# Kernel optimization log

Hardware: AMD Instinct MI355X
Metric: run time of the kernel (lower is better)

The kernel has to match this reference:

```python
import jax, jax.numpy as jnp
import numpy as np

B, N, XDIM, EDIM, H = 4, 256, 256, 128, 8
DF = XDIM // H


def _linear_params(key, din, dout):
    k1, k2 = jax.random.split(key)
    s = 1.0 / np.sqrt(din)
    W = jax.random.uniform(k1, (din, dout), minval=-s, maxval=s, dtype=jnp.float32)
    b = jax.random.uniform(k2, (dout,), minval=-s, maxval=s, dtype=jnp.float32)
    return W, b


def setup_inputs() -> dict:
    key = jax.random.key(0)
    ks = jax.random.split(key, 9)
    x = jax.random.normal(ks[0], (B, N, XDIM), dtype=jnp.float32)
    e = jax.random.normal(ks[1], (B, N, N, EDIM), dtype=jnp.float32)
    Wq, bq = _linear_params(ks[2], XDIM, XDIM)
    Wk, bk = _linear_params(ks[3], XDIM, XDIM)
    Wv, bv = _linear_params(ks[4], XDIM, XDIM)
    Wem, bem = _linear_params(ks[5], EDIM, XDIM)  # e_mul
    Wea, bea = _linear_params(ks[6], EDIM, XDIM)  # e_add
    Wxo, bxo = _linear_params(ks[7], XDIM, XDIM)  # x_out
    Weo, beo = _linear_params(ks[8], XDIM, EDIM)  # e_out
    return {"x": x, "e": e, "Wq": Wq, "bq": bq, "Wk": Wk, "bk": bk,
            "Wv": Wv, "bv": bv, "Wem": Wem, "bem": bem, "Wea": Wea, "bea": bea,
            "Wxo": Wxo, "bxo": bxo, "Weo": Weo, "beo": beo}


def reference(x, e, Wq, bq, Wk, bk, Wv, bv, Wem, bem, Wea, bea, Wxo, bxo, Weo, beo):
    Bq, Nq, _ = x.shape
    # per-node projections -> [B, N, H, DF]
    Q = (x @ Wq + bq).reshape(Bq, Nq, H, DF)
    K = (x @ Wk + bk).reshape(Bq, Nq, H, DF)
    V = (x @ Wv + bv).reshape(Bq, Nq, H, DF)
    # broadcasted outer product: Y[b,i,j,h,d] = Q[b,i,h,d] * K[b,j,h,d] / sqrt(DF)
    Y = Q[:, :, None] * K[:, None] * (1.0 / np.sqrt(DF))  # [B,N,N,H,DF]
    # edge modulation
    E1 = (e @ Wem + bem).reshape(Bq, Nq, Nq, H, DF)
    E2 = (e @ Wea + bea).reshape(Bq, Nq, Nq, H, DF)
    Y = Y * (E1 + 1.0) + E2
    # new edge features
    newE = Y.reshape(Bq, Nq, Nq, XDIM) @ Weo + beo  # [B,N,N,EDIM]
    # attention: softmax over the FIRST node axis (dim=1), as in the torch code
    attn = jax.nn.softmax(Y, axis=1)  # [B,N,N,H,DF]
    # weighted_V[b,j,h,d] = sum_i attn[b,i,j,h,d] * V[b,j,h,d]
    weighted_V = jnp.sum(attn * V[:, None], axis=1)  # [B,N,H,DF]
    newX = weighted_V.reshape(Bq, Nq, XDIM) @ Wxo + bxo  # [B,N,XDIM]
    return (newX, newE)
```

## Files before the change

### kernel.cpp

```cpp
#include <hip/hip_runtime.h>

#define NN 256
#define XD 256
#define ED 128

typedef __attribute__((ext_vector_type(8))) short short8;
typedef __attribute__((ext_vector_type(4))) float f32x4;

__device__ __forceinline__ unsigned short f2bf(float f) {
    unsigned u = __builtin_bit_cast(unsigned, f);
    u += 0x7FFF + ((u >> 16) & 1);
    return (unsigned short)(u >> 16);
}

#define MFMA16(a, b, c) __builtin_amdgcn_mfma_f32_16x16x32_bf16(a, b, c, 0, 0, 0)

__global__ __launch_bounds__(256) void wprep_kernel(
    const float* __restrict__ Wq, const float* __restrict__ Wk,
    const float* __restrict__ Wv, const float* __restrict__ Wxo,
    const float* __restrict__ Wem, const float* __restrict__ Wea,
    const float* __restrict__ Weo,
    short* __restrict__ WqT, short* __restrict__ WkT,
    short* __restrict__ WvT, short* __restrict__ WxoT,
    short* __restrict__ WemT, short* __restrict__ WeaT,
    short* __restrict__ WeoT)
{
    __shared__ float sT[32][33];
    int blk = blockIdx.x;
    const float* src; short* dst; int din, dout, tile;
    if (blk < 256) {
        int m = blk >> 6; tile = blk & 63; din = 256; dout = 256;
        src = m == 0 ? Wq : (m == 1 ? Wk : (m == 2 ? Wv : Wxo));
        dst = m == 0 ? WqT : (m == 1 ? WkT : (m == 2 ? WvT : WxoT));
    } else if (blk < 320) {
        int m = (blk - 256) >> 5; tile = (blk - 256) & 31; din = 128; dout = 256;
        src = m == 0 ? Wem : Wea; dst = m == 0 ? WemT : WeaT;
    } else {
        tile = blk - 320; din = 256; dout = 128;
        src = Weo; dst = WeoT;
    }
    int ksh = (din == 256) ? 3 : 2;
    int kt = tile & ((1 << ksh) - 1);
    int nt = tile >> ksh;
    int c = threadIdx.x & 31, rbase = threadIdx.x >> 5;
    #pragma unroll
    for (int p = 0; p < 4; ++p) {
        int r = rbase + p * 8;
        sT[r][c] = src[(kt * 32 + r) * dout + nt * 32 + c];
    }
    __syncthreads();
    #pragma unroll
    for (int p = 0; p < 4; ++p) {
        int r = rbase + p * 8;
        dst[(nt * 32 + r) * din + kt * 32 + c] = (short)f2bf(sT[c][r]);
    }
}

__global__ __launch_bounds__(512) void proj_qk_kernel(
    const float* __restrict__ x, const short* __restrict__ WqT,
    const short* __restrict__ WkT, const float* __restrict__ bq,
    const float* __restrict__ bk, float* __restrict__ Qs,
    float* __restrict__ KT)
{
    __shared__ unsigned short sX[64 * 264];
    const int blk = blockIdx.x;
    const int mtile = blk >> 1;
    const int mat   = blk & 1;
    const int tid = threadIdx.x, wave = tid >> 6, lane = tid & 63;
    const int quad = lane >> 4, l16 = lane & 15;

    {
        const float4* src4 = (const float4*)(x + (size_t)mtile * 64 * XD);
        #pragma unroll
        for (int it = 0; it < 8; ++it) {
            int idx4 = tid + it * 512;
            float4 v = src4[idx4];
            int elem = idx4 * 4, row = elem >> 8, col = elem & 255;
            short4 p = make_short4((short)f2bf(v.x), (short)f2bf(v.y),
                                   (short)f2bf(v.z), (short)f2bf(v.w));
            *(short4*)&sX[row * 264 + col] = p;
        }
    }
    __syncthreads();

    const short* WT   = mat ? WkT : WqT;
    const float* bias = mat ? bk : bq;
    const int c0 = wave * 32;

    f32x4 acc[4][2] = {};
    for (int ks = 0; ks < 8; ++ks) {
        short8 bfrag[2];
        #pragma unroll
        for (int ct = 0; ct < 2; ++ct)
            bfrag[ct] = *(const short8*)&WT[(c0 + ct * 16 + l16) * 256 + ks * 32 + quad * 8];
        #pragma unroll
        for (int mt = 0; mt < 4; ++mt) {
            short8 a = *(const short8*)&sX[(mt * 16 + l16) * 264 + ks * 32 + quad * 8];
            acc[mt][0] = MFMA16(a, bfrag[0], acc[mt][0]);
            acc[mt][1] = MFMA16(a, bfrag[1], acc[mt][1]);
        }
    }

    if (mat == 0) {
        #pragma unroll
        for (int mt = 0; mt < 4; ++mt)
            #pragma unroll
            for (int ct = 0; ct < 2; ++ct) {
                int cc = c0 + ct * 16 + l16;
                float bb = bias[cc];
                #pragma unroll
                for (int r = 0; r < 4; ++r)
                    Qs[(size_t)(mtile * 64 + mt * 16 + quad * 4 + r) * 256 + cc] =
                        (acc[mt][ct][r] + bb) * 0.17677669529663687f;
            }
    } else {
        int b = mtile >> 2, j0p = (mtile & 3) * 64;
        #pragma unroll
        for (int mt = 0; mt < 4; ++mt)
            #pragma unroll
            for (int ct = 0; ct < 2; ++ct) {
                int cc = c0 + ct * 16 + l16;
                float bb = bias[cc];
                f32x4 st;
                #pragma unroll
                for (int r = 0; r < 4; ++r) st[r] = acc[mt][ct][r] + bb;
                *(f32x4*)&KT[(size_t)(b * 256 + cc) * 256 + j0p + mt * 16 + quad * 4] = st;
            }
    }
}

__global__ __launch_bounds__(512) void proj_vx_kernel(
    const float* __restrict__ x, const short* __restrict__ WvT,
    const float* __restrict__ bv, const short* __restrict__ WxoT,
    const float* __restrict__ bxo, float* __restrict__ outX)
{
    __shared__ unsigned short sX[64 * 264];
    __shared__ unsigned short sV[64 * 264];
    const int mtile = blockIdx.x;
    const int tid = threadIdx.x, wave = tid >> 6, lane = tid & 63;
    const int quad = lane >> 4, l16 = lane & 15;

    {
        const float4* src4 = (const float4*)(x + (size_t)mtile * 64 * XD);
        #pragma unroll
        for (int it = 0; it < 8; ++it) {
            int idx4 = tid + it * 512;
            float4 v = src4[idx4];
            int elem = idx4 * 4, row = elem >> 8, col = elem & 255;
            short4 p = make_short4((short)f2bf(v.x), (short)f2bf(v.y),
                                   (short)f2bf(v.z), (short)f2bf(v.w));
            *(short4*)&sX[row * 264 + col] = p;
        }
    }
    __syncthreads();

    const int c0 = wave * 32;
    f32x4 acc[4][2] = {};
    for (int ks = 0; ks < 8; ++ks) {
        short8 bfrag[2];
        #pragma unroll
        for (int ct = 0; ct < 2; ++ct)
            bfrag[ct] = *(const short8*)&WvT[(c0 + ct * 16 + l16) * 256 + ks * 32 + quad * 8];
        #pragma unroll
        for (int mt = 0; mt < 4; ++mt) {
            short8 a = *(const short8*)&sX[(mt * 16 + l16) * 264 + ks * 32 + quad * 8];
            acc[mt][0] = MFMA16(a, bfrag[0], acc[mt][0]);
            acc[mt][1] = MFMA16(a, bfrag[1], acc[mt][1]);
        }
    }
    #pragma unroll
    for (int mt = 0; mt < 4; ++mt)
        #pragma unroll
        for (int ct = 0; ct < 2; ++ct) {
            int cc = c0 + ct * 16 + l16;
            float bb = bv[cc];
            #pragma unroll
            for (int r = 0; r < 4; ++r)
                sV[(mt * 16 + quad * 4 + r) * 264 + cc] = f2bf(acc[mt][ct][r] + bb);
        }
    __syncthreads();

    f32x4 acc2[4][2] = {};
    for (int ks = 0; ks < 8; ++ks) {
        short8 bfrag[2];
        #pragma unroll
        for (int ct = 0; ct < 2; ++ct)
            bfrag[ct] = *(const short8*)&WxoT[(c0 + ct * 16 + l16) * 256 + ks * 32 + quad * 8];
        #pragma unroll
        for (int mt = 0; mt < 4; ++mt) {
            short8 a = *(const short8*)&sV[(mt * 16 + l16) * 264 + ks * 32 + quad * 8];
            acc2[mt][0] = MFMA16(a, bfrag[0], acc2[mt][0]);
            acc2[mt][1] = MFMA16(a, bfrag[1], acc2[mt][1]);
        }
    }
    #pragma unroll
    for (int mt = 0; mt < 4; ++mt)
        #pragma unroll
        for (int ct = 0; ct < 2; ++ct) {
            int cc = c0 + ct * 16 + l16;
            float bb = bxo[cc];
            #pragma unroll
            for (int r = 0; r < 4; ++r)
                outX[(size_t)(mtile * 64 + mt * 16 + quad * 4 + r) * 256 + cc] =
                    acc2[mt][ct][r] + bb;
        }
}

__global__ __launch_bounds__(256, 3) void fused_edge_kernel(
    const float* __restrict__ e, const float* __restrict__ Qs,
    const float* __restrict__ KT, const short* __restrict__ WemT,
    const short* __restrict__ WeaT, const short* __restrict__ WeoT,
    const float* __restrict__ bem, const float* __restrict__ bea,
    const float* __restrict__ beo, float* __restrict__ outE)
{
    __shared__ unsigned short sE[64 * 140];
    __shared__ unsigned short sY[64 * 268];

    const int blk  = blockIdx.x;
    const int jq   = blk & 3;
    const int i    = (blk >> 2) & 255;
    const int b    = blk >> 10;
    const int j0   = jq * 64;
    const int tid  = threadIdx.x;
    const int wave = tid >> 6;
    const int lane = tid & 63;
    const int quad = lane >> 4;
    const int l16  = lane & 15;

    {
        const float4* src4 = (const float4*)(e + (size_t)((b * NN + i) * NN + j0) * ED);
        #pragma unroll
        for (int it = 0; it < 8; ++it) {
            int idx4 = tid + it * 256;
            float4 v = src4[idx4];
            int elem = idx4 * 4, row = elem >> 7, col = elem & 127;
            short4 p = make_short4((short)f2bf(v.x), (short)f2bf(v.y),
                                   (short)f2bf(v.z), (short)f2bf(v.w));
            *(short4*)&sE[row * 140 + col] = p;
        }
    }

    const float* Qrow = Qs + (size_t)(b * NN + i) * XD;
    float bo[2];
    #pragma unroll
    for (int ct = 0; ct < 2; ++ct) bo[ct] = beo[wave * 32 + ct * 16 + l16];

    __syncthreads();

    #pragma unroll
    for (int p = 0; p < 2; ++p) {
        const int c0 = wave * 32 + p * 128;
        float qsv[2], bmv[2], bav[2];
        int ktA[2];
        #pragma unroll
        for (int ct = 0; ct < 2; ++ct) {
            int cc = c0 + ct * 16 + l16;
            qsv[ct] = Qrow[cc];
            bmv[ct] = bem[cc] + 1.0f;
            bav[ct] = bea[cc];
            ktA[ct] = (b * 256 + cc) * 256 + j0 + quad * 4;
        }
        short8 B1[4][2], B2[4][2];
        #pragma unroll
        for (int ks = 0; ks < 4; ++ks)
            #pragma unroll
            for (int ct = 0; ct < 2; ++ct) {
                int n = c0 + ct * 16 + l16;
                B1[ks][ct] = *(const short8*)&WemT[n * 128 + ks * 32 + quad * 8];
                B2[ks][ct] = *(const short8*)&WeaT[n * 128 + ks * 32 + quad * 8];
            }
        #pragma unroll
        for (int mc = 0; mc < 4; ++mc) {
            const int m0 = mc * 16;
            f32x4 aE1[2] = {}, aE2[2] = {};
            #pragma unroll
            for (int ks = 0; ks < 4; ++ks) {
                short8 a = *(const short8*)&sE[(m0 + l16) * 140 + ks * 32 + quad * 8];
                aE1[0] = MFMA16(a, B1[ks][0], aE1[0]);
                aE1[1] = MFMA16(a, B1[ks][1], aE1[1]);
                aE2[0] = MFMA16(a, B2[ks][0], aE2[0]);
                aE2[1] = MFMA16(a, B2[ks][1], aE2[1]);
            }
            #pragma unroll
            for (int ct = 0; ct < 2; ++ct) {
                f32x4 kv = *(const f32x4*)&KT[ktA[ct] + m0];
                int cc = c0 + ct * 16 + l16;
                #pragma unroll
                for (int r = 0; r < 4; ++r) {
                    float y = qsv[ct] * kv[r] * (aE1[ct][r] + bmv[ct])
                              + (aE2[ct][r] + bav[ct]);
                    sY[(m0 + quad * 4 + r) * 268 + cc] = f2bf(y);
                }
            }
        }
    }
    __syncthreads();

    short8 B3[8][2];
    #pragma unroll
    for (int ks = 0; ks < 8; ++ks)
        #pragma unroll
        for (int ct = 0; ct < 2; ++ct)
            B3[ks][ct] = *(const short8*)&WeoT[(wave * 32 + ct * 16 + l16) * 256 + ks * 32 + quad * 8];
    f32x4 acc2[4][2] = {};
    #pragma unroll
    for (int ks = 0; ks < 8; ++ks) {
        #pragma unroll
        for (int mt = 0; mt < 4; ++mt) {
            short8 a = *(const short8*)&sY[(mt * 16 + l16) * 268 + ks * 32 + quad * 8];
            acc2[mt][0] = MFMA16(a, B3[ks][0], acc2[mt][0]);
            acc2[mt][1] = MFMA16(a, B3[ks][1], acc2[mt][1]);
        }
    }
    float* outBase = outE + (size_t)((b * NN + i) * NN + j0) * ED;
    #pragma unroll
    for (int mt = 0; mt < 4; ++mt)
        #pragma unroll
        for (int ct = 0; ct < 2; ++ct) {
            int col = wave * 32 + ct * 16 + l16;
            #pragma unroll
            for (int r = 0; r < 4; ++r)
                outBase[(size_t)(mt * 16 + quad * 4 + r) * ED + col] = acc2[mt][ct][r] + bo[ct];
        }
}

extern "C" void kernel_launch(void* const* d_in, const int* in_sizes, int n_in,
                              void* d_out, int out_size, void* d_ws, size_t ws_size,
                              hipStream_t stream)
{
    const float* x   = (const float*)d_in[0];
    const float* e   = (const float*)d_in[1];
    const float* Wq  = (const float*)d_in[2];
    const float* bq  = (const float*)d_in[3];
    const float* Wk  = (const float*)d_in[4];
    const float* bk  = (const float*)d_in[5];
    const float* Wv  = (const float*)d_in[6];
    const float* bv  = (const float*)d_in[7];
    const float* Wem = (const float*)d_in[8];
    const float* bem = (const float*)d_in[9];
    const float* Wea = (const float*)d_in[10];
    const float* bea = (const float*)d_in[11];
    const float* Wxo = (const float*)d_in[12];
    const float* bxo = (const float*)d_in[13];
    const float* Weo = (const float*)d_in[14];
    const float* beo = (const float*)d_in[15];

    float* outX = (float*)d_out;
    float* outE = (float*)d_out + 262144;

    float* Qs   = (float*)d_ws;
    float* KT   = Qs + 262144;
    short* WqT  = (short*)(KT + 262144);
    short* WkT  = WqT + 65536;
    short* WvT  = WkT + 65536;
    short* WxoT = WvT + 65536;
    short* WemT = WxoT + 65536;
    short* WeaT = WemT + 32768;
    short* WeoT = WeaT + 32768;

    hipLaunchKernelGGL(wprep_kernel, dim3(352), dim3(256), 0, stream,
                       Wq, Wk, Wv, Wxo, Wem, Wea, Weo,
                       WqT, WkT, WvT, WxoT, WemT, WeaT, WeoT);
    hipLaunchKernelGGL(proj_qk_kernel, dim3(32), dim3(512), 0, stream,
                       x, WqT, WkT, bq, bk, Qs, KT);
    hipLaunchKernelGGL(proj_vx_kernel, dim3(16), dim3(512), 0, stream,
                       x, WvT, bv, WxoT, bxo, outX);
    hipLaunchKernelGGL(fused_edge_kernel, dim3(4096), dim3(256), 0, stream,
                       e, Qs, KT, WemT, WeaT, WeoT, bem, bea, beo, outE);
}
```

Before: 366.2 us.

## Keep edge tiles in registers with transposed MFMA and permuted Weo

Restructures the fused edge kernel so each wave loads its own 32 edge rows straight into MFMA B-fragment registers, computes the E1/E2 projections transposed (weights as the A operand), and feeds the resulting Y fragments directly into the output projection. A permuted bf16 copy of Weo is prepared so those register fragments line up with the k-order the second MFMA expects. This removes both shared-memory staging buffers and the block barriers, and K is now stored row-major instead of transposed. In exchange, every wave re-reads WemT/WeaT/WeoP from global or L2 per chunk, register pressure rises with 16 output accumulators, and the grid halves to 2048 blocks.

Result: slower. 518.1 us (+41.5%).

```diff
diff --git a/kernel.cpp b/kernel.cpp
--- a/kernel.cpp
+++ b/kernel.cpp
@@ -14,6 +14,15 @@
 }
 
 #define MFMA16(a, b, c) __builtin_amdgcn_mfma_f32_16x16x32_bf16(a, b, c, 0, 0, 0)
+
+__device__ __forceinline__ short8 pack8(float4 a, float4 b) {
+    short8 r;
+    r[0] = (short)f2bf(a.x); r[1] = (short)f2bf(a.y);
+    r[2] = (short)f2bf(a.z); r[3] = (short)f2bf(a.w);
+    r[4] = (short)f2bf(b.x); r[5] = (short)f2bf(b.y);
+    r[6] = (short)f2bf(b.z); r[7] = (short)f2bf(b.w);
+    return r;
+}
 
 __global__ __launch_bounds__(256) void wprep_kernel(
     const float* __restrict__ Wq, const float* __restrict__ Wk,
@@ -23,21 +32,31 @@
     short* __restrict__ WqT, short* __restrict__ WkT,
     short* __restrict__ WvT, short* __restrict__ WxoT,
     short* __restrict__ WemT, short* __restrict__ WeaT,
-    short* __restrict__ WeoT)
+    short* __restrict__ WeoP)
 {
     __shared__ float sT[32][33];
     int blk = blockIdx.x;
+    if (blk >= 320) {
+        int t = (blk - 320) * 256 + threadIdx.x;
+        int n = t >> 6;
+        int kk0 = (t & 63) * 4;
+        #pragma unroll
+        for (int r = 0; r < 4; ++r) {
+            int kk = kk0 + r;
+            int sigma = (((kk >> 5) * 2 + ((kk >> 2) & 1)) << 4) +
+                        (((kk >> 3) & 3) << 2) + (kk & 3);
+            WeoP[n * 256 + kk] = (short)f2bf(Weo[sigma * 128 + n]);
+        }
+        return;
+    }
     const float* src; short* dst; int din, dout, tile;
     if (blk < 256) {
         int m = blk >> 6; tile = blk & 63; din = 256; dout = 256;
         src = m == 0 ? Wq : (m == 1 ? Wk : (m == 2 ? Wv : Wxo));
         dst = m == 0 ? WqT : (m == 1 ? WkT : (m == 2 ? WvT : WxoT));
-    } else if (blk < 320) {
+    } else {
         int m = (blk - 256) >> 5; tile = (blk - 256) & 31; din = 128; dout = 256;
         src = m == 0 ? Wem : Wea; dst = m == 0 ? WemT : WeaT;
-    } else {
-        tile = blk - 320; din = 256; dout = 128;
-        src = Weo; dst = WeoT;
     }
     int ksh = (din == 256) ? 3 : 2;
     int kt = tile & ((1 << ksh) - 1);
@@ -60,7 +79,7 @@
     const float* __restrict__ x, const short* __restrict__ WqT,
     const short* __restrict__ WkT, const float* __restrict__ bq,
     const float* __restrict__ bk, float* __restrict__ Qs,
-    float* __restrict__ KT)
+    float* __restrict__ Kb)
 {
     __shared__ unsigned short sX[64 * 264];
     const int blk = blockIdx.x;
@@ -85,6 +104,8 @@
 
     const short* WT   = mat ? WkT : WqT;
     const float* bias = mat ? bk : bq;
+    float* out        = mat ? Kb : Qs;
+    const float scale = mat ? 1.0f : 0.17677669529663687f;
     const int c0 = wave * 32;
 
     f32x4 acc[4][2] = {};
@@ -100,33 +121,17 @@
             acc[mt][1] = MFMA16(a, bfrag[1], acc[mt][1]);
         }
     }
-
-    if (mat == 0) {
-        #pragma unroll
-        for (int mt = 0; mt < 4; ++mt)
-            #pragma unroll
-            for (int ct = 0; ct < 2; ++ct) {
-                int cc = c0 + ct * 16 + l16;
-                float bb = bias[cc];
-                #pragma unroll
-                for (int r = 0; r < 4; ++r)
-                    Qs[(size_t)(mtile * 64 + mt * 16 + quad * 4 + r) * 256 + cc] =
-                        (acc[mt][ct][r] + bb) * 0.17677669529663687f;
-            }
-    } else {
-        int b = mtile >> 2, j0p = (mtile & 3) * 64;
-        #pragma unroll
-        for (int mt = 0; mt < 4; ++mt)
-            #pragma unroll
-            for (int ct = 0; ct < 2; ++ct) {
-                int cc = c0 + ct * 16 + l16;
-                float bb = bias[cc];
-                f32x4 st;
-                #pragma unroll
-                for (int r = 0; r < 4; ++r) st[r] = acc[mt][ct][r] + bb;
-                *(f32x4*)&KT[(size_t)(b * 256 + cc) * 256 + j0p + mt * 16 + quad * 4] = st;
-            }
-    }
+    #pragma unroll
+    for (int mt = 0; mt < 4; ++mt)
+        #pragma unroll
+        for (int ct = 0; ct < 2; ++ct) {
+            int cc = c0 + ct * 16 + l16;
+            float bb = bias[cc];
+            #pragma unroll
+            for (int r = 0; r < 4; ++r)
+                out[(size_t)(mtile * 64 + mt * 16 + quad * 4 + r) * 256 + cc] =
+                    (acc[mt][ct][r] + bb) * scale;
+        }
 }
 
 __global__ __launch_bounds__(512) void proj_vx_kernel(
@@ -208,120 +213,97 @@
 
 __global__ __launch_bounds__(256, 3) void fused_edge_kernel(
     const float* __restrict__ e, const float* __restrict__ Qs,
-    const float* __restrict__ KT, const short* __restrict__ WemT,
-    const short* __restrict__ WeaT, const short* __restrict__ WeoT,
+    const float* __restrict__ Kb, const short* __restrict__ WemT,
+    const short* __restrict__ WeaT, const short* __restrict__ WeoP,
     const float* __restrict__ bem, const float* __restrict__ bea,
     const float* __restrict__ beo, float* __restrict__ outE)
 {
-    __shared__ unsigned short sE[64 * 140];
-    __shared__ unsigned short sY[64 * 268];
-
     const int blk  = blockIdx.x;
-    const int jq   = blk & 3;
-    const int i    = (blk >> 2) & 255;
-    const int b    = blk >> 10;
-    const int j0   = jq * 64;
-    const int tid  = threadIdx.x;
-    const int wave = tid >> 6;
-    const int lane = tid & 63;
-    const int quad = lane >> 4;
+    const int jh   = blk & 1;
+    const int i    = (blk >> 1) & 255;
+    const int b    = blk >> 9;
+    const int wave = threadIdx.x >> 6;
+    const int lane = threadIdx.x & 63;
+    const int q    = lane >> 4;
     const int l16  = lane & 15;
-
+    const int j0   = jh * 128 + wave * 32;
+
+    short8 Be[2][4];
     {
-        const float4* src4 = (const float4*)(e + (size_t)((b * NN + i) * NN + j0) * ED);
-        #pragma unroll
-        for (int it = 0; it < 8; ++it) {
-            int idx4 = tid + it * 256;
-            float4 v = src4[idx4];
-            int elem = idx4 * 4, row = elem >> 7, col = elem & 127;
-            short4 p = make_short4((short)f2bf(v.x), (short)f2bf(v.y),
-                                   (short)f2bf(v.z), (short)f2bf(v.w));
-            *(short4*)&sE[row * 140 + col] = p;
+        const size_t erow = ((size_t)(b * NN + i) * NN + j0 + l16) * ED;
+        #pragma unroll
+        for (int nt = 0; nt < 2; ++nt) {
+            const float* ep = e + erow + nt * 16 * ED + q * 8;
+            #pragma unroll
+            for (int ks = 0; ks < 4; ++ks) {
+                float4 lo = *(const float4*)(ep + ks * 32);
+                float4 hi = *(const float4*)(ep + ks * 32 + 4);
+                Be[nt][ks] = pack8(lo, hi);
+            }
         }
     }
 
     const float* Qrow = Qs + (size_t)(b * NN + i) * XD;
-    float bo[2];
-    #pragma unroll
-    for (int ct = 0; ct < 2; ++ct) bo[ct] = beo[wave * 32 + ct * 16 + l16];
-
-    __syncthreads();
-
-    #pragma unroll
-    for (int p = 0; p < 2; ++p) {
-        const int c0 = wave * 32 + p * 128;
-        float qsv[2], bmv[2], bav[2];
-        int ktA[2];
-        #pragma unroll
-        for (int ct = 0; ct < 2; ++ct) {
-            int cc = c0 + ct * 16 + l16;
-            qsv[ct] = Qrow[cc];
-            bmv[ct] = bem[cc] + 1.0f;
-            bav[ct] = bea[cc];
-            ktA[ct] = (b * 256 + cc) * 256 + j0 + quad * 4;
-        }
-        short8 B1[4][2], B2[4][2];
-        #pragma unroll
-        for (int ks = 0; ks < 4; ++ks)
-            #pragma unroll
-            for (int ct = 0; ct < 2; ++ct) {
-                int n = c0 + ct * 16 + l16;
-                B1[ks][ct] = *(const short8*)&WemT[n * 128 + ks * 32 + quad * 8];
-                B2[ks][ct] = *(const short8*)&WeaT[n * 128 + ks * 32 + quad * 8];
+    const size_t krow0 = ((size_t)b * NN + j0 + l16) * XD;
+
+    f32x4 acc2[8][2] = {};
+
+    #pragma unroll
+    for (int c = 0; c < 8; ++c) {
+        short8 B2[2];
+        #pragma unroll
+        for (int h = 0; h < 2; ++h) {
+            const int mt = 2 * c + h;
+            const int xb = mt * 16 + q * 4;
+            f32x4 a1[2] = {}, a2[2] = {};
+            #pragma unroll
+            for (int ks = 0; ks < 4; ++ks) {
+                short8 Am = *(const short8*)&WemT[(mt * 16 + l16) * 128 + ks * 32 + q * 8];
+                short8 Aa = *(const short8*)&WeaT[(mt * 16 + l16) * 128 + ks * 32 + q * 8];
+                a1[0] = MFMA16(Am, Be[0][ks], a1[0]);
+                a1[1] = MFMA16(Am, Be[1][ks], a1[1]);
+                a2[0] = MFMA16(Aa, Be[0][ks], a2[0]);
+                a2[1] = MFMA16(Aa, Be[1][ks], a2[1]);
             }
-        #pragma unroll
-        for (int mc = 0; mc < 4; ++mc) {
-            const int m0 = mc * 16;
-            f32x4 aE1[2] = {}, aE2[2] = {};
-            #pragma unroll
-            for (int ks = 0; ks < 4; ++ks) {
-                short8 a = *(const short8*)&sE[(m0 + l16) * 140 + ks * 32 + quad * 8];
-                aE1[0] = MFMA16(a, B1[ks][0], aE1[0]);
-                aE1[1] = MFMA16(a, B1[ks][1], aE1[1]);
-                aE2[0] = MFMA16(a, B2[ks][0], aE2[0]);
-                aE2[1] = MFMA16(a, B2[ks][1], aE2[1]);
+            float4 qs = *(const float4*)&Qrow[xb];
+            float4 bm = *(const float4*)&bem[xb];
+            float4 ba = *(const float4*)&bea[xb];
+            #pragma unroll
+            for (int nt = 0; nt < 2; ++nt) {
+                float4 kv = *(const float4*)&Kb[krow0 + nt * 16 * XD + xb];
+                float y0 = qs.x * kv.x * (a1[nt][0] + bm.x + 1.0f) + a2[nt][0] + ba.x;
+                float y1 = qs.y * kv.y * (a1[nt][1] + bm.y + 1.0f) + a2[nt][1] + ba.y;
+                float y2 = qs.z * kv.z * (a1[nt][2] + bm.z + 1.0f) + a2[nt][2] + ba.z;
+                float y3 = qs.w * kv.w * (a1[nt][3] + bm.w + 1.0f) + a2[nt][3] + ba.w;
+                B2[nt][h * 4 + 0] = (short)f2bf(y0);
+                B2[nt][h * 4 + 1] = (short)f2bf(y1);
+                B2[nt][h * 4 + 2] = (short)f2bf(y2);
+                B2[nt][h * 4 + 3] = (short)f2bf(y3);
             }
-            #pragma unroll
-            for (int ct = 0; ct < 2; ++ct) {
-                f32x4 kv = *(const f32x4*)&KT[ktA[ct] + m0];
-                int cc = c0 + ct * 16 + l16;
-                #pragma unroll
-                for (int r = 0; r < 4; ++r) {
-                    float y = qsv[ct] * kv[r] * (aE1[ct][r] + bmv[ct])
-                              + (aE2[ct][r] + bav[ct]);
-                    sY[(m0 + quad * 4 + r) * 268 + cc] = f2bf(y);
-                }
-            }
-        }
-    }
-    __syncthreads();
-
-    short8 B3[8][2];
-    #pragma unroll
-    for (int ks = 0; ks < 8; ++ks)
-        #pragma unroll
-        for (int ct = 0; ct < 2; ++ct)
-            B3[ks][ct] = *(const short8*)&WeoT[(wave * 32 + ct * 16 + l16) * 256 + ks * 32 + quad * 8];
-    f32x4 acc2[4][2] = {};
-    #pragma unroll
-    for (int ks = 0; ks < 8; ++ks) {
-        #pragma unroll
-        for (int mt = 0; mt < 4; ++mt) {
-            short8 a = *(const short8*)&sY[(mt * 16 + l16) * 268 + ks * 32 + quad * 8];
-            acc2[mt][0] = MFMA16(a, B3[ks][0], acc2[mt][0]);
-            acc2[mt][1] = MFMA16(a, B3[ks][1], acc2[mt][1]);
-        }
-    }
-    float* outBase = outE + (size_t)((b * NN + i) * NN + j0) * ED;
-    #pragma unroll
-    for (int mt = 0; mt < 4; ++mt)
-        #pragma unroll
-        for (int ct = 0; ct < 2; ++ct) {
-            int col = wave * 32 + ct * 16 + l16;
-            #pragma unroll
-            for (int r = 0; r < 4; ++r)
-                outBase[(size_t)(mt * 16 + quad * 4 + r) * ED + col] = acc2[mt][ct][r] + bo[ct];
-        }
+        }
+        #pragma unroll
+        for (int m2 = 0; m2 < 8; ++m2) {
+            short8 A2 = *(const short8*)&WeoP[(m2 * 16 + l16) * 256 + c * 32 + q * 8];
+            acc2[m2][0] = MFMA16(A2, B2[0], acc2[m2][0]);
+            acc2[m2][1] = MFMA16(A2, B2[1], acc2[m2][1]);
+        }
+    }
+
+    float* outBase = outE + ((size_t)(b * NN + i) * NN + j0 + l16) * ED;
+    #pragma unroll
+    for (int m2 = 0; m2 < 8; ++m2) {
+        const int ed = m2 * 16 + q * 4;
+        float4 bo = *(const float4*)&beo[ed];
+        #pragma unroll
+        for (int nt = 0; nt < 2; ++nt) {
+            float4 st;
+            st.x = acc2[m2][nt][0] + bo.x;
+            st.y = acc2[m2][nt][1] + bo.y;
+            st.z = acc2[m2][nt][2] + bo.z;
+            st.w = acc2[m2][nt][3] + bo.w;
+            *(float4*)(outBase + (size_t)nt * 16 * ED + ed) = st;
+        }
+    }
 }
 
 extern "C" void kernel_launch(void* const* d_in, const int* in_sizes, int n_in,
@@ -349,22 +331,22 @@
     float* outE = (float*)d_out + 262144;
 
     float* Qs   = (float*)d_ws;
-    float* KT   = Qs + 262144;
-    short* WqT  = (short*)(KT + 262144);
+    float* Kb   = Qs + 262144;
+    short* WqT  = (short*)(Kb + 262144);
     short* WkT  = WqT + 65536;
     short* WvT  = WkT + 65536;
     short* WxoT = WvT + 65536;
     short* WemT = WxoT + 65536;
     short* WeaT = WemT + 32768;
-    short* WeoT = WeaT + 32768;
+    short* WeoP = WeaT + 32768;
 
     hipLaunchKernelGGL(wprep_kernel, dim3(352), dim3(256), 0, stream,
                        Wq, Wk, Wv, Wxo, Wem, Wea, Weo,
-                       WqT, WkT, WvT, WxoT, WemT, WeaT, WeoT);
+                       WqT, WkT, WvT, WxoT, WemT, WeaT, WeoP);
     hipLaunchKernelGGL(proj_qk_kernel, dim3(32), dim3(512), 0, stream,
-                       x, WqT, WkT, bq, bk, Qs, KT);
+                       x, WqT, WkT, bq, bk, Qs, Kb);
     hipLaunchKernelGGL(proj_vx_kernel, dim3(16), dim3(512), 0, stream,
                        x, WvT, bv, WxoT, bxo, outX);
-    hipLaunchKernelGGL(fused_edge_kernel, dim3(4096), dim3(256), 0, stream,
-                       e, Qs, KT, WemT, WeaT, WeoT, bem, bea, beo, outE);
-}
+    hipLaunchKernelGGL(fused_edge_kernel, dim3(2048), dim3(256), 0, stream,
+                       e, Qs, Kb, WemT, WeaT, WeoP, bem, bea, beo, outE);
+}
```

## Loop over j-tiles per block with register prefetch of next e tile and bf16 K

Applied to the files above, without the earlier changes.

The edge kernel now runs one block per (b,i) and loops over four 64-row j tiles. The next tile's e values and K slices are prefetched into registers while the current tile is computed, so global load latency overlaps with MFMA work. K is stored as bf16 instead of fp32, which halves its traffic. In exchange the grid shrinks to 1024 blocks, occupancy is lowered to 2 blocks per CU with more register pressure, and rounding K to bf16 adds precision error.

New measurement: 434.1 us. 18.5% more time.

```diff
diff --git a/kernel.cpp b/kernel.cpp
--- a/kernel.cpp
+++ b/kernel.cpp
@@ -11,6 +11,10 @@
     unsigned u = __builtin_bit_cast(unsigned, f);
     u += 0x7FFF + ((u >> 16) & 1);
     return (unsigned short)(u >> 16);
+}
+__device__ __forceinline__ float bf2f(unsigned short h) {
+    unsigned u = ((unsigned)h) << 16;
+    return __builtin_bit_cast(float, u);
 }
 
 #define MFMA16(a, b, c) __builtin_amdgcn_mfma_f32_16x16x32_bf16(a, b, c, 0, 0, 0)
@@ -60,7 +64,7 @@
     const float* __restrict__ x, const short* __restrict__ WqT,
     const short* __restrict__ WkT, const float* __restrict__ bq,
     const float* __restrict__ bk, float* __restrict__ Qs,
-    float* __restrict__ KT)
+    unsigned short* __restrict__ Kbf)
 {
     __shared__ unsigned short sX[64 * 264];
     const int blk = blockIdx.x;
@@ -121,10 +125,12 @@
             for (int ct = 0; ct < 2; ++ct) {
                 int cc = c0 + ct * 16 + l16;
                 float bb = bias[cc];
-                f32x4 st;
-                #pragma unroll
-                for (int r = 0; r < 4; ++r) st[r] = acc[mt][ct][r] + bb;
-                *(f32x4*)&KT[(size_t)(b * 256 + cc) * 256 + j0p + mt * 16 + quad * 4] = st;
+                short4 st;
+                st.x = (short)f2bf(acc[mt][ct][0] + bb);
+                st.y = (short)f2bf(acc[mt][ct][1] + bb);
+                st.z = (short)f2bf(acc[mt][ct][2] + bb);
+                st.w = (short)f2bf(acc[mt][ct][3] + bb);
+                *(short4*)&Kbf[(size_t)(b * 256 + cc) * 256 + j0p + mt * 16 + quad * 4] = st;
             }
     }
 }
@@ -206,122 +212,159 @@
         }
 }
 
-__global__ __launch_bounds__(256, 3) void fused_edge_kernel(
+__global__ __launch_bounds__(256, 2) void fused_edge_kernel(
     const float* __restrict__ e, const float* __restrict__ Qs,
-    const float* __restrict__ KT, const short* __restrict__ WemT,
+    const unsigned short* __restrict__ Kbf, const short* __restrict__ WemT,
     const short* __restrict__ WeaT, const short* __restrict__ WeoT,
     const float* __restrict__ bem, const float* __restrict__ bea,
     const float* __restrict__ beo, float* __restrict__ outE)
 {
     __shared__ unsigned short sE[64 * 140];
-    __shared__ unsigned short sY[64 * 268];
+    __shared__ unsigned short sY[64 * 264];
 
     const int blk  = blockIdx.x;
-    const int jq   = blk & 3;
-    const int i    = (blk >> 2) & 255;
-    const int b    = blk >> 10;
-    const int j0   = jq * 64;
+    const int i    = blk & 255;
+    const int b    = blk >> 8;
     const int tid  = threadIdx.x;
     const int wave = tid >> 6;
     const int lane = tid & 63;
-    const int quad = lane >> 4;
+    const int q    = lane >> 4;
     const int l16  = lane & 15;
-
-    {
-        const float4* src4 = (const float4*)(e + (size_t)((b * NN + i) * NN + j0) * ED);
+    const int c0w  = wave * 32;
+
+    const float* eBase = e + (size_t)((b * NN + i) * NN) * ED;
+    const unsigned short* kB = Kbf + (size_t)b * 256 * 256;
+    const float* Qrow = Qs + (size_t)(b * NN + i) * XD;
+
+    float qsv[2][2], bmv[2][2], bav[2][2], bo[2];
+    #pragma unroll
+    for (int p = 0; p < 2; ++p)
+        #pragma unroll
+        for (int ct = 0; ct < 2; ++ct) {
+            int cc = p * 128 + c0w + ct * 16 + l16;
+            qsv[p][ct] = Qrow[cc];
+            bmv[p][ct] = bem[cc] + 1.0f;
+            bav[p][ct] = bea[cc];
+        }
+    #pragma unroll
+    for (int ct = 0; ct < 2; ++ct) bo[ct] = beo[wave * 32 + ct * 16 + l16];
+
+    float4 f[8];
+    #pragma unroll
+    for (int it = 0; it < 8; ++it)
+        f[it] = ((const float4*)eBase)[tid + it * 256];
+    short4 kpf[16];
+    #pragma unroll
+    for (int p = 0; p < 2; ++p)
+        #pragma unroll
+        for (int mc = 0; mc < 4; ++mc)
+            #pragma unroll
+            for (int ct = 0; ct < 2; ++ct) {
+                int cc = p * 128 + c0w + ct * 16 + l16;
+                kpf[p * 8 + mc * 2 + ct] =
+                    *(const short4*)&kB[(size_t)cc * 256 + mc * 16 + q * 4];
+            }
+
+    for (int t = 0; t < 4; ++t) {
+        const int j0  = t * 64;
+        const int j0n = ((t + 1) & 3) * 64;
+
         #pragma unroll
         for (int it = 0; it < 8; ++it) {
             int idx4 = tid + it * 256;
-            float4 v = src4[idx4];
             int elem = idx4 * 4, row = elem >> 7, col = elem & 127;
-            short4 p = make_short4((short)f2bf(v.x), (short)f2bf(v.y),
-                                   (short)f2bf(v.z), (short)f2bf(v.w));
-            *(short4*)&sE[row * 140 + col] = p;
-        }
-    }
-
-    const float* Qrow = Qs + (size_t)(b * NN + i) * XD;
-    float bo[2];
-    #pragma unroll
-    for (int ct = 0; ct < 2; ++ct) bo[ct] = beo[wave * 32 + ct * 16 + l16];
-
-    __syncthreads();
-
-    #pragma unroll
-    for (int p = 0; p < 2; ++p) {
-        const int c0 = wave * 32 + p * 128;
-        float qsv[2], bmv[2], bav[2];
-        int ktA[2];
-        #pragma unroll
-        for (int ct = 0; ct < 2; ++ct) {
-            int cc = c0 + ct * 16 + l16;
-            qsv[ct] = Qrow[cc];
-            bmv[ct] = bem[cc] + 1.0f;
-            bav[ct] = bea[cc];
-            ktA[ct] = (b * 256 + cc) * 256 + j0 + quad * 4;
-        }
-        short8 B1[4][2], B2[4][2];
-        #pragma unroll
-        for (int ks = 0; ks < 4; ++ks)
+            short4 pk = make_short4((short)f2bf(f[it].x), (short)f2bf(f[it].y),
+                                    (short)f2bf(f[it].z), (short)f2bf(f[it].w));
+            *(short4*)&sE[row * 140 + col] = pk;
+        }
+        __syncthreads();
+
+        {
+            const float4* eN = (const float4*)(eBase + (size_t)j0n * ED);
+            #pragma unroll
+            for (int it = 0; it < 8; ++it)
+                f[it] = eN[tid + it * 256];
+        }
+
+        #pragma unroll
+        for (int p = 0; p < 2; ++p) {
+            const int c0 = p * 128 + c0w;
+            short8 B1[4][2], B2[4][2];
+            #pragma unroll
+            for (int ks = 0; ks < 4; ++ks)
+                #pragma unroll
+                for (int ct = 0; ct < 2; ++ct) {
+                    int n = c0 + ct * 16 + l16;
+                    B1[ks][ct] = *(const short8*)&WemT[n * 128 + ks * 32 + q * 8];
+                    B2[ks][ct] = *(const short8*)&WeaT[n * 128 + ks * 32 + q * 8];
+                }
+            #pragma unroll
+            for (int mc = 0; mc < 4; ++mc) {
+                const int m0 = mc * 16;
+                f32x4 aE1[2] = {}, aE2[2] = {};
+                #pragma unroll
+                for (int ks = 0; ks < 4; ++ks) {
+                    short8 a = *(const short8*)&sE[(m0 + l16) * 140 + ks * 32 + q * 8];
+                    aE1[0] = MFMA16(a, B1[ks][0], aE1[0]);
+                    aE1[1] = MFMA16(a, B1[ks][1], aE1[1]);
+                    aE2[0] = MFMA16(a, B2[ks][0], aE2[0]);
+                    aE2[1] = MFMA16(a, B2[ks][1], aE2[1]);
+                }
+                #pragma unroll
+                for (int ct = 0; ct < 2; ++ct) {
+                    short4 kv4 = kpf[p * 8 + mc * 2 + ct];
+                    float kv[4] = { bf2f((unsigned short)kv4.x), bf2f((unsigned short)kv4.y),
+                                    bf2f((unsigned short)kv4.z), bf2f((unsigned short)kv4.w) };
+                    int cc = c0 + ct * 16 + l16;
+                    #pragma unroll
+                    for (int r = 0; r < 4; ++r) {
+                        float y = qsv[p][ct] * kv[r] * (aE1[ct][r] + bmv[p][ct])
+                                  + (aE2[ct][r] + bav[p][ct]);
+                        sY[(m0 + q * 4 + r) * 264 + cc] = f2bf(y);
+                    }
+                }
+            }
+        }
+        __syncthreads();
+
+        #pragma unroll
+        for (int p = 0; p < 2; ++p)
+            #pragma unroll
+            for (int mc = 0; mc < 4; ++mc)
+                #pragma unroll
+                for (int ct = 0; ct < 2; ++ct) {
+                    int cc = p * 128 + c0w + ct * 16 + l16;
+                    kpf[p * 8 + mc * 2 + ct] =
+                        *(const short4*)&kB[(size_t)cc * 256 + j0n + mc * 16 + q * 4];
+                }
+
+        short8 B3[8][2];
+        #pragma unroll
+        for (int ks = 0; ks < 8; ++ks)
+            #pragma unroll
+            for (int ct = 0; ct < 2; ++ct)
+                B3[ks][ct] = *(const short8*)&WeoT[(wave * 32 + ct * 16 + l16) * 256 + ks * 32 + q * 8];
+        f32x4 acc2[4][2] = {};
+        #pragma unroll
+        for (int ks = 0; ks < 8; ++ks) {
+            #pragma unroll
+            for (int mt = 0; mt < 4; ++mt) {
+                short8 a = *(const short8*)&sY[(mt * 16 + l16) * 264 + ks * 32 + q * 8];
+                acc2[mt][0] = MFMA16(a, B3[ks][0], acc2[mt][0]);
+                acc2[mt][1] = MFMA16(a, B3[ks][1], acc2[mt][1]);
+            }
+        }
+        float* outBase = outE + (size_t)((b * NN + i) * NN + j0) * ED;
+        #pragma unroll
+        for (int mt = 0; mt < 4; ++mt)
             #pragma unroll
             for (int ct = 0; ct < 2; ++ct) {
-                int n = c0 + ct * 16 + l16;
-                B1[ks][ct] = *(const short8*)&WemT[n * 128 + ks * 32 + quad * 8];
-                B2[ks][ct] = *(const short8*)&WeaT[n * 128 + ks * 32 + quad * 8];
-            }
-        #pragma unroll
-        for (int mc = 0; mc < 4; ++mc) {
-            const int m0 = mc * 16;
-            f32x4 aE1[2] = {}, aE2[2] = {};
-            #pragma unroll
-            for (int ks = 0; ks < 4; ++ks) {
-                short8 a = *(const short8*)&sE[(m0 + l16) * 140 + ks * 32 + quad * 8];
-                aE1[0] = MFMA16(a, B1[ks][0], aE1[0]);
-                aE1[1] = MFMA16(a, B1[ks][1], aE1[1]);
-                aE2[0] = MFMA16(a, B2[ks][0], aE2[0]);
-                aE2[1] = MFMA16(a, B2[ks][1], aE2[1]);
-            }
-            #pragma unroll
-            for (int ct = 0; ct < 2; ++ct) {
-                f32x4 kv = *(const f32x4*)&KT[ktA[ct] + m0];
-                int cc = c0 + ct * 16 + l16;
-                #pragma unroll
-                for (int r = 0; r < 4; ++r) {
-                    float y = qsv[ct] * kv[r] * (aE1[ct][r] + bmv[ct])
-                              + (aE2[ct][r] + bav[ct]);
-                    sY[(m0 + quad * 4 + r) * 268 + cc] = f2bf(y);
-                }
-            }
-        }
-    }
-    __syncthreads();
-
-    short8 B3[8][2];
-    #pragma unroll
-    for (int ks = 0; ks < 8; ++ks)
-        #pragma unroll
-        for (int ct = 0; ct < 2; ++ct)
-            B3[ks][ct] = *(const short8*)&WeoT[(wave * 32 + ct * 16 + l16) * 256 + ks * 32 + quad * 8];
-    f32x4 acc2[4][2] = {};
-    #pragma unroll
-    for (int ks = 0; ks < 8; ++ks) {
-        #pragma unroll
-        for (int mt = 0; mt < 4; ++mt) {
-            short8 a = *(const short8*)&sY[(mt * 16 + l16) * 268 + ks * 32 + quad * 8];
-            acc2[mt][0] = MFMA16(a, B3[ks][0], acc2[mt][0]);
-            acc2[mt][1] = MFMA16(a, B3[ks][1], acc2[mt][1]);
-        }
-    }
-    float* outBase = outE + (size_t)((b * NN + i) * NN + j0) * ED;
-    #pragma unroll
-    for (int mt = 0; mt < 4; ++mt)
-        #pragma unroll
-        for (int ct = 0; ct < 2; ++ct) {
-            int col = wave * 32 + ct * 16 + l16;
-            #pragma unroll
-            for (int r = 0; r < 4; ++r)
-                outBase[(size_t)(mt * 16 + quad * 4 + r) * ED + col] = acc2[mt][ct][r] + bo[ct];
-        }
+                int col = wave * 32 + ct * 16 + l16;
+                #pragma unroll
+                for (int r = 0; r < 4; ++r)
+                    outBase[(size_t)(mt * 16 + q * 4 + r) * ED + col] = acc2[mt][ct][r] + bo[ct];
+            }
+    }
 }
 
 extern "C" void kernel_launch(void* const* d_in, const int* in_sizes, int n_in,
@@ -348,9 +391,9 @@
     float* outX = (float*)d_out;
     float* outE = (float*)d_out + 262144;
 
-    float* Qs   = (float*)d_ws;
-    float* KT   = Qs + 262144;
-    short* WqT  = (short*)(KT + 262144);
+    float* Qs           = (float*)d_ws;
+    unsigned short* Kbf = (unsigned short*)(Qs + 262144);
+    short* WqT  = (short*)(Kbf + 262144);
     short* WkT  = WqT + 65536;
     short* WvT  = WkT + 65536;
     short* WxoT = WvT + 65536;
@@ -362,9 +405,9 @@
                        Wq, Wk, Wv, Wxo, Wem, Wea, Weo,
                        WqT, WkT, WvT, WxoT, WemT, WeaT, WeoT);
     hipLaunchKernelGGL(proj_qk_kernel, dim3(32), dim3(512), 0, stream,
-                       x, WqT, WkT, bq, bk, Qs, KT);
+                       x, WqT, WkT, bq, bk, Qs, Kbf);
     hipLaunchKernelGGL(proj_vx_kernel, dim3(16), dim3(512), 0, stream,
                        x, WvT, bv, WxoT, bxo, outX);
-    hipLaunchKernelGGL(fused_edge_kernel, dim3(4096), dim3(256), 0, stream,
-                       e, Qs, KT, WemT, WeaT, WeoT, bem, bea, beo, outE);
-}
+    hipLaunchKernelGGL(fused_edge_kernel, dim3(1024), dim3(256), 0, stream,
+                       e, Qs, Kbf, WemT, WeaT, WeoT, bem, bea, beo, outE);
+}
```
